# Kernel optimization log

Measured on AMD Instinct MI355X. Metric: run time of the kernel, lower is better.

Reference implementation:

```python
import jax, jax.numpy as jnp
import numpy as np

B, L, D, H = 2, 2048, 1024, 16
DK = D // H  # head_dim = 64


def setup_inputs() -> dict:
    key = jax.random.key(0)
    ks = jax.random.split(key, 12)
    init = lambda k, shape, fan_in: jax.random.uniform(k, shape, jnp.float32, -1.0, 1.0) / np.sqrt(fan_in)
    inp = {
        "query": jax.random.normal(ks[0], (B, L, D), jnp.float32),
        "key": jax.random.normal(ks[1], (B, L, D), jnp.float32),
        "value": jax.random.normal(ks[2], (B, L, D), jnp.float32),
        # causal mask [B, 1, L, L], True = attend
        "mask": jnp.broadcast_to(jnp.tril(jnp.ones((L, L), bool))[None, None], (B, 1, L, L)),
        "wq": init(ks[3], (D, D), D), "bq": jnp.zeros((D,), jnp.float32),
        "wk": init(ks[4], (D, D), D), "bk": jnp.zeros((D,), jnp.float32),
        "wv": init(ks[5], (D, D), D), "bv": jnp.zeros((D,), jnp.float32),
        "wo": init(ks[6], (D, D), D), "bo": jnp.zeros((D,), jnp.float32),
    }
    return inp


def reference(query, key, value, mask, wq, bq, wk, bk, wv, bv, wo, bo):
    b, l, d = query.shape
    split = lambda x: x.reshape(b, l, H, DK).transpose(0, 2, 1, 3)  # B H L dk
    Q = split(query @ wq + bq)
    K = split(key @ wk + bk)
    V = split(value @ wv + bv)
    scores = jnp.einsum("bhqd,bhkd->bhqk", Q, K) / jnp.sqrt(jnp.float32(DK))
    probs = jax.nn.softmax(scores, axis=-1, where=mask)  # masked-out rows contribute 0
    attn = jnp.einsum("bhqk,bhkd->bhqd", probs, V)
    out = attn.transpose(0, 2, 1, 3).reshape(b, l, d)  # B L D
    return out @ wo + bo
```

## Files before the change

### kernel.cpp

```cpp
#include <hip/hip_runtime.h>
#include <hip/hip_bf16.h>

typedef __bf16 bf16x8 __attribute__((ext_vector_type(8)));
typedef __bf16 bf16x4 __attribute__((ext_vector_type(4)));
typedef float floatx4 __attribute__((ext_vector_type(4)));

constexpr int Bn  = 2;
constexpr int Ln  = 2048;
constexpr int Dn  = 1024;
constexpr int Hn  = 16;
constexpr int DKn = 64;
constexpr int Mn  = Bn * Ln;

__device__ __forceinline__ void gload_lds16(const void* g, void* l) {
  __builtin_amdgcn_global_load_lds(
      (const __attribute__((address_space(1))) void*)g,
      (__attribute__((address_space(3))) void*)l, 16, 0, 0);
}

__global__ __launch_bounds__(256) void cvt3(
    const float* __restrict__ q, const float* __restrict__ k,
    const float* __restrict__ v, __hip_bfloat16* __restrict__ dst)
{
  const float* src = blockIdx.z == 0 ? q : blockIdx.z == 1 ? k : v;
  __hip_bfloat16* d = dst + (size_t)blockIdx.z * Mn * Dn;
  const int i = blockIdx.x * 256 + threadIdx.x;
  const float4 a = ((const float4*)src)[i * 2];
  const float4 b = ((const float4*)src)[i * 2 + 1];
  bf16x8 o;
  o[0] = (__bf16)a.x; o[1] = (__bf16)a.y; o[2] = (__bf16)a.z; o[3] = (__bf16)a.w;
  o[4] = (__bf16)b.x; o[5] = (__bf16)b.y; o[6] = (__bf16)b.z; o[7] = (__bf16)b.w;
  ((bf16x8*)d)[i] = o;
}

__global__ __launch_bounds__(256) void transpose4(
    const float* __restrict__ wq, const float* __restrict__ wk,
    const float* __restrict__ wv, const float* __restrict__ wo,
    __hip_bfloat16* __restrict__ out)
{
  const float* src = blockIdx.z == 0 ? wq : blockIdx.z == 1 ? wk
                   : blockIdx.z == 2 ? wv : wo;
  __hip_bfloat16* dst = out + (size_t)blockIdx.z * Dn * Dn;
  __shared__ __bf16 tile[32][33];
  const int tx = threadIdx.x, ty = threadIdx.y;
  const int x = blockIdx.x * 32 + tx;
  const int y = blockIdx.y * 32 + ty;
  for (int i = 0; i < 32; i += 8)
    tile[ty + i][tx] = (__bf16)src[(size_t)(y + i) * Dn + x];
  __syncthreads();
  const int x2 = blockIdx.y * 32 + tx;
  const int y2 = blockIdx.x * 32 + ty;
  for (int i = 0; i < 32; i += 8)
    ((__bf16*)dst)[(size_t)(y2 + i) * Dn + x2] = tile[tx][ty + i];
}

__global__ __launch_bounds__(256) void gemm_qkv(
    const __hip_bfloat16* __restrict__ Abf,
    const __hip_bfloat16* __restrict__ wT,
    const float* __restrict__ bq, const float* __restrict__ bk,
    const float* __restrict__ bv,
    __hip_bfloat16* __restrict__ Qp, __hip_bfloat16* __restrict__ Kp,
    __hip_bfloat16* __restrict__ Vt)
{
  constexpr int BK = 32;
  __shared__ __bf16 As[128][BK];
  __shared__ __bf16 Ws[128][BK];
  const int z = blockIdx.z;
  const __hip_bfloat16* A  = Abf + (size_t)z * Mn * Dn;
  const __hip_bfloat16* WT = wT  + (size_t)z * Dn * Dn;
  const float* bias = z == 0 ? bq : z == 1 ? bk : bv;

  const int m0 = blockIdx.x * 128;
  const int n0 = blockIdx.y * 128;
  const int tid  = threadIdx.x;
  const int lane = tid & 63;
  const int wave = tid >> 6;
  const int quad = lane >> 4;
  const int l16  = lane & 15;
  const int wm = (wave >> 1) * 64;
  const int wn = (wave & 1) * 64;
  const int srow = tid >> 2;
  const int scol = (tid & 3) * 8;

  floatx4 acc[4][4];
  for (int i = 0; i < 4; i++)
    for (int j = 0; j < 4; j++)
      acc[i][j] = (floatx4){0.f, 0.f, 0.f, 0.f};

  for (int k0 = 0; k0 < Dn; k0 += BK) {
    for (int half = 0; half < 2; half++) {
      gload_lds16(&A [(size_t)(m0 + srow + half * 64) * Dn + k0 + scol],
                  &As[srow + half * 64][scol]);
      gload_lds16(&WT[(size_t)(n0 + srow + half * 64) * Dn + k0 + scol],
                  &Ws[srow + half * 64][scol]);
    }
    __syncthreads();
    bf16x8 af[4], wf[4];
    for (int i = 0; i < 4; i++) af[i] = *(const bf16x8*)&As[wm + i * 16 + l16][quad * 8];
    for (int j = 0; j < 4; j++) wf[j] = *(const bf16x8*)&Ws[wn + j * 16 + l16][quad * 8];
    if (z == 2) {
      for (int i = 0; i < 4; i++)
        for (int j = 0; j < 4; j++)
          acc[i][j] = __builtin_amdgcn_mfma_f32_16x16x32_bf16(af[i], wf[j], acc[i][j], 0, 0, 0);
    } else {
      for (int i = 0; i < 4; i++)
        for (int j = 0; j < 4; j++)
          acc[i][j] = __builtin_amdgcn_mfma_f32_16x16x32_bf16(wf[j], af[i], acc[i][j], 0, 0, 0);
    }
    __syncthreads();
  }

  if (z == 2) {
    for (int j = 0; j < 4; j++) {
      const int n = n0 + wn + j * 16 + l16;
      const float bvv = bias[n];
      const int h = n >> 6, dk = n & 63;
      for (int i = 0; i < 4; i++) {
        const int m = m0 + wm + i * 16 + quad * 4;
        const int b = m >> 11, li = m & (Ln - 1);
        bf16x4 pk;
        for (int r = 0; r < 4; r++) pk[r] = (__bf16)(acc[i][j][r] + bvv);
        *(bf16x4*)&Vt[(((size_t)(b * Hn + h)) * DKn + dk) * Ln + li] = pk;
      }
    }
  } else {
    __hip_bfloat16* out = z == 0 ? Qp : Kp;
    for (int j = 0; j < 4; j++) {
      const int nq = n0 + wn + j * 16 + quad * 4;
      const float4 b4 = *(const float4*)&bias[nq];
      const int h = nq >> 6, dk = nq & 63;
      for (int i = 0; i < 4; i++) {
        const int m = m0 + wm + i * 16 + l16;
        const int b = m >> 11, li = m & (Ln - 1);
        bf16x4 pk;
        pk[0] = (__bf16)(acc[i][j][0] + b4.x);
        pk[1] = (__bf16)(acc[i][j][1] + b4.y);
        pk[2] = (__bf16)(acc[i][j][2] + b4.z);
        pk[3] = (__bf16)(acc[i][j][3] + b4.w);
        *(bf16x4*)&out[(((size_t)(b * Hn + h)) * Ln + li) * DKn + dk] = pk;
      }
    }
  }
}

__global__ __launch_bounds__(256) void gemm_out(
    const __hip_bfloat16* __restrict__ A,
    const __hip_bfloat16* __restrict__ WT,
    const float* __restrict__ bias,
    float* __restrict__ out)
{
  constexpr int BK = 32;
  __shared__ __bf16 As[128][BK];
  __shared__ __bf16 Ws[64][BK];
  const int m0 = blockIdx.x * 128;
  const int n0 = blockIdx.y * 64;
  const int tid  = threadIdx.x;
  const int lane = tid & 63;
  const int wave = tid >> 6;
  const int quad = lane >> 4;
  const int l16  = lane & 15;
  const int wm = (wave >> 1) * 64;
  const int wn = (wave & 1) * 32;
  const int srow = tid >> 2;
  const int scol = (tid & 3) * 8;

  floatx4 acc[4][2];
  for (int i = 0; i < 4; i++)
    for (int j = 0; j < 2; j++)
      acc[i][j] = (floatx4){0.f, 0.f, 0.f, 0.f};

  for (int k0 = 0; k0 < Dn; k0 += BK) {
    for (int half = 0; half < 2; half++)
      gload_lds16(&A [(size_t)(m0 + srow + half * 64) * Dn + k0 + scol],
                  &As[srow + half * 64][scol]);
    gload_lds16(&WT[(size_t)(n0 + srow) * Dn + k0 + scol], &Ws[srow][scol]);
    __syncthreads();
    bf16x8 af[4], wf[2];
    for (int i = 0; i < 4; i++) af[i] = *(const bf16x8*)&As[wm + i * 16 + l16][quad * 8];
    for (int j = 0; j < 2; j++) wf[j] = *(const bf16x8*)&Ws[wn + j * 16 + l16][quad * 8];
    for (int i = 0; i < 4; i++)
      for (int j = 0; j < 2; j++)
        acc[i][j] = __builtin_amdgcn_mfma_f32_16x16x32_bf16(af[i], wf[j], acc[i][j], 0, 0, 0);
    __syncthreads();
  }

  for (int j = 0; j < 2; j++) {
    const int n = n0 + wn + j * 16 + l16;
    const float bvv = bias[n];
    for (int i = 0; i < 4; i++)
      for (int r = 0; r < 4; r++) {
        const int m = m0 + wm + i * 16 + quad * 4 + r;
        out[(size_t)m * Dn + n] = acc[i][j][r] + bvv;
      }
  }
}

__global__ __launch_bounds__(256) void attn_flash(
    const __hip_bfloat16* __restrict__ Qp,
    const __hip_bfloat16* __restrict__ Kp,
    const __hip_bfloat16* __restrict__ Vt,
    __hip_bfloat16* __restrict__ attn)
{
  const int bh   = blockIdx.x;
  const int qt   = (gridDim.y - 1 - blockIdx.y);
  const int tid  = threadIdx.x;
  const int wave = tid >> 6;
  const int lane = tid & 63;
  const int quad = lane >> 4;
  const int l16  = lane & 15;
  const int qb0  = qt * 128;
  const int qw   = qb0 + wave * 32;

  const __hip_bfloat16* Qh = Qp + (size_t)bh * Ln * DKn;
  const __hip_bfloat16* Kh = Kp + (size_t)bh * Ln * DKn;
  const __hip_bfloat16* Vh = Vt + (size_t)bh * DKn * Ln;

  __shared__ __align__(16) __bf16 Ks[2][64][64];
  __shared__ __align__(16) __bf16 Vs[2][64][64];
  __shared__ __align__(16) __bf16 Plds[4][2][16][72];

  bf16x8 qf[2][2];
  for (int m = 0; m < 2; m++)
    for (int dd = 0; dd < 2; dd++)
      qf[m][dd] = *(const bf16x8*)&Qh[(size_t)(qw + m * 16 + l16) * DKn + dd * 32 + quad * 8];

  floatx4 o[2][4];
  for (int m = 0; m < 2; m++)
    for (int t = 0; t < 4; t++) o[m][t] = (floatx4){0.f, 0.f, 0.f, 0.f};
  float lp[2] = {0.f, 0.f};

  const int srow8 = lane >> 3;
  const int gch   = (lane & 7) ^ srow8;
  const int xs    = (l16 & 7);

  auto stage = [&](int buf, int kt) {
    for (int s = 0; s < 2; s++) {
      const int u = wave + s * 4;
      gload_lds16(Kh + (size_t)(kt + u * 8 + srow8) * DKn + gch * 8,
                  &Ks[buf][u * 8][0] + (size_t)lane * 8);
      gload_lds16(Vh + (size_t)(u * 8 + srow8) * Ln + kt + gch * 8,
                  &Vs[buf][u * 8][0] + (size_t)lane * 8);
    }
  };

  const int kend_w = qw + 32;
  const int kend_b = qb0 + 128;
  stage(0, 0);
  int buf = 0;
  for (int kt = 0; kt < kend_b; kt += 64, buf ^= 1) {
    __syncthreads();
    if (kt + 64 < kend_b) stage(buf ^ 1, kt + 64);
    if (kt < kend_w) {
      floatx4 s[2][4];
      for (int m = 0; m < 2; m++)
        for (int sub = 0; sub < 4; sub++) s[m][sub] = (floatx4){0.f, 0.f, 0.f, 0.f};
      for (int sub = 0; sub < 4; sub++)
        for (int dd = 0; dd < 2; dd++) {
          bf16x8 kf = *(const bf16x8*)&Ks[buf][sub * 16 + l16][((dd * 4 + quad) ^ xs) * 8];
          s[0][sub] = __builtin_amdgcn_mfma_f32_16x16x32_bf16(kf, qf[0][dd], s[0][sub], 0, 0, 0);
          s[1][sub] = __builtin_amdgcn_mfma_f32_16x16x32_bf16(kf, qf[1][dd], s[1][sub], 0, 0, 0);
        }
      bf16x8 vf[4][2];
      for (int t = 0; t < 4; t++)
        for (int kc = 0; kc < 2; kc++)
          vf[t][kc] = *(const bf16x8*)&Vs[buf][t * 16 + l16][((kc * 4 + quad) ^ xs) * 8];

      for (int m = 0; m < 2; m++) {
        const bool needmask = (kt + 64 > qw + m * 16);
        const int qg = qw + m * 16 + l16;
        for (int sub = 0; sub < 4; sub++) {
          bf16x4 pk;
          for (int r = 0; r < 4; r++) {
            float sv = s[m][sub][r];
            if (needmask && (kt + sub * 16 + quad * 4 + r > qg)) sv = -1e30f;
            const float e = __builtin_exp2f(__builtin_fmaf(sv, 0.18033688f, -11.5415603f));
            lp[m] += e;
            pk[r] = (__bf16)e;
          }
          *(bf16x4*)&Plds[wave][m][l16][sub * 16 + quad * 4] = pk;
        }
      }
      __asm__ volatile("s_waitcnt lgkmcnt(0)" ::: "memory");

      bf16x8 pf[2][2];
      for (int m = 0; m < 2; m++)
        for (int kc = 0; kc < 2; kc++)
          pf[m][kc] = *(const bf16x8*)&Plds[wave][m][l16][kc * 32 + quad * 8];
      for (int m = 0; m < 2; m++)
        for (int t = 0; t < 4; t++)
          for (int kc = 0; kc < 2; kc++)
            o[m][t] = __builtin_amdgcn_mfma_f32_16x16x32_bf16(pf[m][kc], vf[t][kc], o[m][t], 0, 0, 0);
    }
  }

  const int b = bh >> 4, h = bh & 15;
  for (int m = 0; m < 2; m++) {
    float lf = lp[m];
    lf += __shfl_xor(lf, 16);
    lf += __shfl_xor(lf, 32);
    for (int r = 0; r < 4; r++) {
      const float lr = __shfl(lf, (lane & 48) | (quad * 4 + r));
      const float inv = 1.0f / lr;
      const int ql = qw + m * 16 + quad * 4 + r;
      const size_t base = ((size_t)b * Ln + ql) * Dn + h * DKn;
      for (int t = 0; t < 4; t++)
        attn[base + t * 16 + l16] = __float2bfloat16(o[m][t][r] * inv);
    }
  }
}

extern "C" void kernel_launch(void* const* d_in, const int* in_sizes, int n_in,
                              void* d_out, int out_size, void* d_ws, size_t ws_size,
                              hipStream_t stream) {
  const float* query = (const float*)d_in[0];
  const float* key_  = (const float*)d_in[1];
  const float* value = (const float*)d_in[2];
  const float* wq = (const float*)d_in[4];
  const float* bq = (const float*)d_in[5];
  const float* wk = (const float*)d_in[6];
  const float* bk = (const float*)d_in[7];
  const float* wv = (const float*)d_in[8];
  const float* bv = (const float*)d_in[9];
  const float* wo = (const float*)d_in[10];
  const float* bo = (const float*)d_in[11];

  const size_t T   = (size_t)Mn * Dn;
  const size_t WSZ = (size_t)Dn * Dn;
  __hip_bfloat16* Abf  = (__hip_bfloat16*)d_ws;
  __hip_bfloat16* Qp   = Abf + 3 * T;
  __hip_bfloat16* Kp   = Qp + T;
  __hip_bfloat16* Vt   = Kp + T;
  __hip_bfloat16* wT   = Vt + T;
  __hip_bfloat16* attn = Abf;

  transpose4<<<dim3(Dn / 32, Dn / 32, 4), dim3(32, 8), 0, stream>>>(wq, wk, wv, wo, wT);
  cvt3<<<dim3((int)(T / 2048), 1, 3), 256, 0, stream>>>(query, key_, value, Abf);
  gemm_qkv<<<dim3(Mn / 128, Dn / 128, 3), 256, 0, stream>>>(Abf, wT, bq, bk, bv, Qp, Kp, Vt);
  attn_flash<<<dim3(Bn * Hn, Ln / 128), 256, 0, stream>>>(Qp, Kp, Vt, attn);
  gemm_out<<<dim3(Mn / 128, Dn / 64), 256, 0, stream>>>(attn, wT + 3 * WSZ, bo, (float*)d_out);
}
```

Before: 271.8 us.

## Pair causal query tiles per block and merge prep kernels

The attention kernel now runs 128-thread blocks, each handling two 64-row query tiles (qt and 31-qt). This balances causal work evenly across blocks and removes the old per-wave idle iterations. The PV MFMA operands are swapped so each lane holds a contiguous run of output columns, which allows vectorized bf16x4 stores. The weight transpose and input conversion kernels are merged into one launch to save launch overhead, at the cost of idle blocks in the transpose z-slices.

```diff
diff --git a/kernel.cpp b/kernel.cpp
--- a/kernel.cpp
+++ b/kernel.cpp
@@ -18,40 +18,39 @@
       (__attribute__((address_space(3))) void*)l, 16, 0, 0);
 }
 
-__global__ __launch_bounds__(256) void cvt3(
+__global__ __launch_bounds__(256) void prep(
     const float* __restrict__ q, const float* __restrict__ k,
-    const float* __restrict__ v, __hip_bfloat16* __restrict__ dst)
-{
-  const float* src = blockIdx.z == 0 ? q : blockIdx.z == 1 ? k : v;
-  __hip_bfloat16* d = dst + (size_t)blockIdx.z * Mn * Dn;
-  const int i = blockIdx.x * 256 + threadIdx.x;
-  const float4 a = ((const float4*)src)[i * 2];
-  const float4 b = ((const float4*)src)[i * 2 + 1];
-  bf16x8 o;
-  o[0] = (__bf16)a.x; o[1] = (__bf16)a.y; o[2] = (__bf16)a.z; o[3] = (__bf16)a.w;
-  o[4] = (__bf16)b.x; o[5] = (__bf16)b.y; o[6] = (__bf16)b.z; o[7] = (__bf16)b.w;
-  ((bf16x8*)d)[i] = o;
-}
-
-__global__ __launch_bounds__(256) void transpose4(
+    const float* __restrict__ v,
     const float* __restrict__ wq, const float* __restrict__ wk,
     const float* __restrict__ wv, const float* __restrict__ wo,
-    __hip_bfloat16* __restrict__ out)
+    __hip_bfloat16* __restrict__ Abf, __hip_bfloat16* __restrict__ wT)
 {
-  const float* src = blockIdx.z == 0 ? wq : blockIdx.z == 1 ? wk
-                   : blockIdx.z == 2 ? wv : wo;
-  __hip_bfloat16* dst = out + (size_t)blockIdx.z * Dn * Dn;
+  const int z = blockIdx.z;
   __shared__ __bf16 tile[32][33];
-  const int tx = threadIdx.x, ty = threadIdx.y;
-  const int x = blockIdx.x * 32 + tx;
-  const int y = blockIdx.y * 32 + ty;
-  for (int i = 0; i < 32; i += 8)
-    tile[ty + i][tx] = (__bf16)src[(size_t)(y + i) * Dn + x];
-  __syncthreads();
-  const int x2 = blockIdx.y * 32 + tx;
-  const int y2 = blockIdx.x * 32 + ty;
-  for (int i = 0; i < 32; i += 8)
-    ((__bf16*)dst)[(size_t)(y2 + i) * Dn + x2] = tile[tx][ty + i];
+  if (z < 3) {
+    const float* src = z == 0 ? q : z == 1 ? k : v;
+    __hip_bfloat16* d = Abf + (size_t)z * Mn * Dn;
+    const int i = blockIdx.x * 256 + threadIdx.x;
+    const float4 a = ((const float4*)src)[i * 2];
+    const float4 b = ((const float4*)src)[i * 2 + 1];
+    bf16x8 o;
+    o[0] = (__bf16)a.x; o[1] = (__bf16)a.y; o[2] = (__bf16)a.z; o[3] = (__bf16)a.w;
+    o[4] = (__bf16)b.x; o[5] = (__bf16)b.y; o[6] = (__bf16)b.z; o[7] = (__bf16)b.w;
+    ((bf16x8*)d)[i] = o;
+  } else {
+    if (blockIdx.x >= 1024) return;
+    const float* src = z == 3 ? wq : z == 4 ? wk : z == 5 ? wv : wo;
+    __hip_bfloat16* dst = wT + (size_t)(z - 3) * Dn * Dn;
+    const int bx = blockIdx.x & 31, by = blockIdx.x >> 5;
+    const int tx = threadIdx.x & 31, ty = threadIdx.x >> 5;
+    const int x = bx * 32 + tx, y = by * 32 + ty;
+    for (int i = 0; i < 32; i += 8)
+      tile[ty + i][tx] = (__bf16)src[(size_t)(y + i) * Dn + x];
+    __syncthreads();
+    const int x2 = by * 32 + tx, y2 = bx * 32 + ty;
+    for (int i = 0; i < 32; i += 8)
+      ((__bf16*)dst)[(size_t)(y2 + i) * Dn + x2] = tile[tx][ty + i];
+  }
 }
 
 __global__ __launch_bounds__(256) void gemm_qkv(
@@ -195,21 +194,19 @@
   }
 }
 
-__global__ __launch_bounds__(256) void attn_flash(
+__global__ __launch_bounds__(128) void attn_flash(
     const __hip_bfloat16* __restrict__ Qp,
     const __hip_bfloat16* __restrict__ Kp,
     const __hip_bfloat16* __restrict__ Vt,
     __hip_bfloat16* __restrict__ attn)
 {
   const int bh   = blockIdx.x;
-  const int qt   = (gridDim.y - 1 - blockIdx.y);
+  const int pA   = blockIdx.y;
   const int tid  = threadIdx.x;
   const int wave = tid >> 6;
   const int lane = tid & 63;
   const int quad = lane >> 4;
   const int l16  = lane & 15;
-  const int qb0  = qt * 128;
-  const int qw   = qb0 + wave * 32;
 
   const __hip_bfloat16* Qh = Qp + (size_t)bh * Ln * DKn;
   const __hip_bfloat16* Kh = Kp + (size_t)bh * Ln * DKn;
@@ -217,40 +214,46 @@
 
   __shared__ __align__(16) __bf16 Ks[2][64][64];
   __shared__ __align__(16) __bf16 Vs[2][64][64];
-  __shared__ __align__(16) __bf16 Plds[4][2][16][72];
-
-  bf16x8 qf[2][2];
-  for (int m = 0; m < 2; m++)
-    for (int dd = 0; dd < 2; dd++)
-      qf[m][dd] = *(const bf16x8*)&Qh[(size_t)(qw + m * 16 + l16) * DKn + dd * 32 + quad * 8];
-
-  floatx4 o[2][4];
-  for (int m = 0; m < 2; m++)
-    for (int t = 0; t < 4; t++) o[m][t] = (floatx4){0.f, 0.f, 0.f, 0.f};
-  float lp[2] = {0.f, 0.f};
+  __shared__ __align__(16) __bf16 Plds[2][2][16][72];
 
   const int srow8 = lane >> 3;
   const int gch   = (lane & 7) ^ srow8;
-  const int xs    = (l16 & 7);
-
-  auto stage = [&](int buf, int kt) {
-    for (int s = 0; s < 2; s++) {
-      const int u = wave + s * 4;
+  const int xs    = l16 & 7;
+  const int b = bh >> 4, h = bh & 15;
+
+  auto stage = [&](int sbuf, int kt) {
+    for (int s = 0; s < 4; s++) {
+      const int u = wave * 4 + s;
       gload_lds16(Kh + (size_t)(kt + u * 8 + srow8) * DKn + gch * 8,
-                  &Ks[buf][u * 8][0] + (size_t)lane * 8);
+                  &Ks[sbuf][u * 8][0] + (size_t)lane * 8);
       gload_lds16(Vh + (size_t)(u * 8 + srow8) * Ln + kt + gch * 8,
-                  &Vs[buf][u * 8][0] + (size_t)lane * 8);
+                  &Vs[sbuf][u * 8][0] + (size_t)lane * 8);
     }
   };
 
-  const int kend_w = qw + 32;
-  const int kend_b = qb0 + 128;
-  stage(0, 0);
-  int buf = 0;
-  for (int kt = 0; kt < kend_b; kt += 64, buf ^= 1) {
-    __syncthreads();
-    if (kt + 64 < kend_b) stage(buf ^ 1, kt + 64);
-    if (kt < kend_w) {
+  for (int half = 0; half < 2; half++) {
+    const int qt = half ? 31 - pA : pA;
+    const int qw = qt * 64 + wave * 32;
+
+    bf16x8 qf[2][2];
+    for (int m = 0; m < 2; m++)
+      for (int dd = 0; dd < 2; dd++)
+        qf[m][dd] = *(const bf16x8*)&Qh[(size_t)(qw + m * 16 + l16) * DKn + dd * 32 + quad * 8];
+
+    floatx4 o[2][4];
+    for (int m = 0; m < 2; m++)
+      for (int t = 0; t < 4; t++) o[m][t] = (floatx4){0.f, 0.f, 0.f, 0.f};
+    float lp[2] = {0.f, 0.f};
+
+    __syncthreads();
+    stage(0, 0);
+    int buf = 0;
+    const int iters = qt + 1;
+    for (int it = 0; it < iters; it++, buf ^= 1) {
+      const int kt = it * 64;
+      __syncthreads();
+      if (it + 1 < iters) stage(buf ^ 1, kt + 64);
+
       floatx4 s[2][4];
       for (int m = 0; m < 2; m++)
         for (int sub = 0; sub < 4; sub++) s[m][sub] = (floatx4){0.f, 0.f, 0.f, 0.f};
@@ -289,22 +292,21 @@
       for (int m = 0; m < 2; m++)
         for (int t = 0; t < 4; t++)
           for (int kc = 0; kc < 2; kc++)
-            o[m][t] = __builtin_amdgcn_mfma_f32_16x16x32_bf16(pf[m][kc], vf[t][kc], o[m][t], 0, 0, 0);
-    }
-  }
-
-  const int b = bh >> 4, h = bh & 15;
-  for (int m = 0; m < 2; m++) {
-    float lf = lp[m];
-    lf += __shfl_xor(lf, 16);
-    lf += __shfl_xor(lf, 32);
-    for (int r = 0; r < 4; r++) {
-      const float lr = __shfl(lf, (lane & 48) | (quad * 4 + r));
-      const float inv = 1.0f / lr;
-      const int ql = qw + m * 16 + quad * 4 + r;
+            o[m][t] = __builtin_amdgcn_mfma_f32_16x16x32_bf16(vf[t][kc], pf[m][kc], o[m][t], 0, 0, 0);
+    }
+
+    for (int m = 0; m < 2; m++) {
+      float lf = lp[m];
+      lf += __shfl_xor(lf, 16);
+      lf += __shfl_xor(lf, 32);
+      const float inv = 1.0f / lf;
+      const int ql = qw + m * 16 + l16;
       const size_t base = ((size_t)b * Ln + ql) * Dn + h * DKn;
-      for (int t = 0; t < 4; t++)
-        attn[base + t * 16 + l16] = __float2bfloat16(o[m][t][r] * inv);
+      for (int t = 0; t < 4; t++) {
+        bf16x4 pk;
+        for (int r = 0; r < 4; r++) pk[r] = (__bf16)(o[m][t][r] * inv);
+        *(bf16x4*)&attn[base + t * 16 + quad * 4] = pk;
+      }
     }
   }
 }
@@ -333,9 +335,8 @@
   __hip_bfloat16* wT   = Vt + T;
   __hip_bfloat16* attn = Abf;
 
-  transpose4<<<dim3(Dn / 32, Dn / 32, 4), dim3(32, 8), 0, stream>>>(wq, wk, wv, wo, wT);
-  cvt3<<<dim3((int)(T / 2048), 1, 3), 256, 0, stream>>>(query, key_, value, Abf);
+  prep<<<dim3(2048, 1, 7), 256, 0, stream>>>(query, key_, value, wq, wk, wv, wo, Abf, wT);
   gemm_qkv<<<dim3(Mn / 128, Dn / 128, 3), 256, 0, stream>>>(Abf, wT, bq, bk, bv, Qp, Kp, Vt);
-  attn_flash<<<dim3(Bn * Hn, Ln / 128), 256, 0, stream>>>(Qp, Kp, Vt, attn);
+  attn_flash<<<dim3(Bn * Hn, Ln / 128), 128, 0, stream>>>(Qp, Kp, Vt, attn);
   gemm_out<<<dim3(Mn / 128, Dn / 64), 256, 0, stream>>>(attn, wT + 3 * WSZ, bo, (float*)d_out);
 }
```

Measured after the change: 283.1 us. 4.2% more time.
